# Kernel tuning notes

Hardware: AMD Instinct MI355X
Metric: run time of the kernel (lower is better)

The kernel has to match this reference:

```python
import jax, jax.numpy as jnp
import numpy as np

POOLED_H = 7
POOLED_W = 7
SPATIAL_SCALE = 0.0625
B, C, H, W = 8, 256, 48, 48
R = 300
IMG = 768  # = H / SPATIAL_SCALE


def setup_inputs() -> dict:
    key = jax.random.key(0)
    k1, k2, k3, k4 = jax.random.split(key, 4)
    features = jax.random.normal(k1, (B, C, H, W), dtype=jnp.float32)
    # rois: (batch_idx, x1, y1, x2, y2) in input-image coords
    bidx = jax.random.randint(k2, (R, 1), 0, B).astype(jnp.float32)
    tl = jax.random.uniform(k3, (R, 2), minval=0.0, maxval=IMG - 64.0)
    wh = jax.random.uniform(k4, (R, 2), minval=32.0, maxval=320.0)
    br = jnp.minimum(tl + wh, IMG - 1.0)
    rois = jnp.concatenate([bidx, tl, br], axis=1).astype(jnp.float32)
    return {"features": features, "rois": rois}


def _hat_integral(x, grid):
    """Integral from -inf to x of the unit hat basis function centered at each
    grid point g (support [g-1, g+1], peak 1, total mass 1).
    x: [..., 1-broadcastable], grid: [G] -> returns [..., G]."""
    t = x[..., None] - (grid - 1.0)
    return jnp.where(
        t <= 0.0, 0.0,
        jnp.where(t <= 1.0, 0.5 * t * t,
                  jnp.where(t <= 2.0, 1.0 - 0.5 * (2.0 - t) ** 2, 1.0)))


def reference(features, rois):
    # Precise RoI Pooling: exact double integral of the bilinear interpolant
    # over each bin, divided by bin area. Bilinear interp (with zero padding
    # outside the map, as in the CUDA PrRoIPoolingGetData) is
    #   f(u,v) = sum_{j,i} feat[j,i] * hat_j(v) * hat_i(u)
    # so the bin integral factorizes into per-axis hat-integral weights.
    Bf, Cf, Hf, Wf = features.shape
    bidx = rois[:, 0].astype(jnp.int32)
    x1 = rois[:, 1] * SPATIAL_SCALE
    y1 = rois[:, 2] * SPATIAL_SCALE
    x2 = rois[:, 3] * SPATIAL_SCALE
    y2 = rois[:, 4] * SPATIAL_SCALE
    roi_w = jnp.maximum(x2 - x1, 0.0)
    roi_h = jnp.maximum(y2 - y1, 0.0)
    bin_w = roi_w / POOLED_W  # [R]
    bin_h = roi_h / POOLED_H

    ph = jnp.arange(POOLED_H, dtype=jnp.float32)
    pw = jnp.arange(POOLED_W, dtype=jnp.float32)
    ya = y1[:, None] + ph[None, :] * bin_h[:, None]  # [R, PH]
    yb = ya + bin_h[:, None]
    xa = x1[:, None] + pw[None, :] * bin_w[:, None]  # [R, PW]
    xb = xa + bin_w[:, None]

    gy = jnp.arange(Hf, dtype=jnp.float32)
    gx = jnp.arange(Wf, dtype=jnp.float32)
    Wy = _hat_integral(yb, gy) - _hat_integral(ya, gy)  # [R, PH, H]
    Wx = _hat_integral(xb, gx) - _hat_integral(xa, gx)  # [R, PW, W]

    feat = features[bidx]  # [R, C, H, W]
    t = jnp.einsum('rpj,rcji->rcpi', Wy, feat)   # integrate over y
    num = jnp.einsum('rqi,rcpi->rcpq', Wx, t)    # integrate over x -> [R,C,PH,PW]

    area = (bin_w * bin_h)[:, None, None, None]  # win_size per ROI
    out = jnp.where(area > 0.0, num / jnp.where(area > 0.0, area, 1.0), 0.0)
    return out
```

## Files before the change

kernel.cpp:

```cpp
#include <hip/hip_runtime.h>


#define PH 7
#define PW 7
#define NBINS 49
#define SCALE 0.0625f
#define CH 256
#define FH 48
#define FW 48
#define RNUM 300
#define PATCHF (23 * 56)
#define RSF 328

__device__ __forceinline__ float hat_int(float x, float g) {
    float t = x - (g - 1.0f);
    if (t <= 0.0f) return 0.0f;
    if (t <= 1.0f) return 0.5f * t * t;
    if (t <= 2.0f) { float u = 2.0f - t; return 1.0f - 0.5f * u * u; }
    return 1.0f;
}

__global__ __launch_bounds__(256, 6)
void prroi_one(const float* __restrict__ feat,
               const float* __restrict__ rois,
               float* __restrict__ out) {
    const int wv   = threadIdx.x >> 6;
    const int lane = threadIdx.x & 63;
    const int r    = blockIdx.y;
    const int cpr  = blockIdx.x * 4 + wv;
    const int c0   = cpr * 2;

    __shared__ float lds[4][PATCHF + RSF];
    float* patch = lds[wv];
    float* rsw   = lds[wv] + PATCHF;

    const float* roi = rois + r * 5;
    const float f0 = roi[0], f1 = roi[1], f2 = roi[2], f3 = roi[3], f4 = roi[4];
    const int   b  = (int)f0;
    const float x1 = f1 * SCALE, y1 = f2 * SCALE;
    const float x2 = f3 * SCALE, y2 = f4 * SCALE;
    const float roi_w = fmaxf(x2 - x1, 0.0f), roi_h = fmaxf(y2 - y1, 0.0f);
    const float bin_w = roi_w / (float)PW, bin_h = roi_h / (float)PH;
    const float area = bin_w * bin_h;
    const float ia   = (area > 0.0f) ? (1.0f / area) : 0.0f;

    const float ylo = fminf(y1, y2), yhi = fmaxf(y1, y2);
    const float xlo = fminf(x1, x2), xhi = fmaxf(x1, x2);
    const int j1 = min(FH - 1, (int)floorf(yhi) + 1);
    const int i1 = min(FW - 1, (int)floorf(xhi) + 1);
    const int J0 = min(max(0, (int)floorf(ylo) - 1), FH - 6);
    const int I0 = min(max(0, (int)floorf(xlo) - 1) & ~3, FW - 8);
    const int JROWS = min(FH - J0, max(j1 - J0 + 1, 6));
    int NI4 = min(((i1 - I0) >> 2) + 1, (FW - I0) >> 2);
    NI4 = max(NI4, 2);

    const int NU = JROWS << 3;
    const float* fb = feat + (size_t)(b * CH + c0) * (FH * FW);
    bool act_[3]; int dst_[3];
    float4 pc0[3], pc1[3];
#pragma unroll
    for (int s = 0; s < 3; ++s) {
        const int u  = lane + (s << 6);
        const int j  = u >> 3, i4 = u & 7;
        const bool a = (u < NU) && (i4 < NI4);
        act_[s] = a;
        dst_[s] = j * 56 + 8 * i4;
        if (a) {
            const float* src = fb + (size_t)(J0 + j) * FW + I0 + 4 * i4;
            pc0[s] = *(const float4*)(src);
            pc1[s] = *(const float4*)(src + FH * FW);
        }
    }

    const int  pwA = lane >> 3, jsl = lane & 7;
    const bool actA = lane < 56;
    float wx0 = 0, wx1 = 0, wx2 = 0, wx3 = 0, wx4 = 0, wx5 = 0;
    int biA = 0;
    if (actA) {
        const float xa = x1 + pwA * bin_w, xb = xa + bin_w;
        const int base = min(max((int)floorf(xa) - 1, I0), I0 + 4 * NI4 - 6);
        biA = base - I0;
        wx0 = hat_int(xb, (float)(base + 0)) - hat_int(xa, (float)(base + 0));
        wx1 = hat_int(xb, (float)(base + 1)) - hat_int(xa, (float)(base + 1));
        wx2 = hat_int(xb, (float)(base + 2)) - hat_int(xa, (float)(base + 2));
        wx3 = hat_int(xb, (float)(base + 3)) - hat_int(xa, (float)(base + 3));
        wx4 = hat_int(xb, (float)(base + 4)) - hat_int(xa, (float)(base + 4));
        wx5 = hat_int(xb, (float)(base + 5)) - hat_int(xa, (float)(base + 5));
    }
    const bool actB = lane < NBINS;
    float wy0 = 0, wy1 = 0, wy2 = 0, wy3 = 0, wy4 = 0, wy5 = 0;
    int pwB = 0, bjB = 0;
    if (actB) {
        const int ph = lane / 7;
        pwB = lane - ph * 7;
        const float ya = y1 + ph * bin_h, yb = ya + bin_h;
        const int base = min(max((int)floorf(ya) - 1, J0), J0 + JROWS - 6);
        bjB = base - J0;
        wy0 = hat_int(yb, (float)(base + 0)) - hat_int(ya, (float)(base + 0));
        wy1 = hat_int(yb, (float)(base + 1)) - hat_int(ya, (float)(base + 1));
        wy2 = hat_int(yb, (float)(base + 2)) - hat_int(ya, (float)(base + 2));
        wy3 = hat_int(yb, (float)(base + 3)) - hat_int(ya, (float)(base + 3));
        wy4 = hat_int(yb, (float)(base + 4)) - hat_int(ya, (float)(base + 4));
        wy5 = hat_int(yb, (float)(base + 5)) - hat_int(ya, (float)(base + 5));
    }

#pragma unroll
    for (int s = 0; s < 3; ++s) {
        if (act_[s]) {
            float* d = patch + dst_[s];
            *(float4*)(d + 0) = make_float4(pc0[s].x, pc1[s].x, pc0[s].y, pc1[s].y);
            *(float4*)(d + 4) = make_float4(pc0[s].z, pc1[s].z, pc0[s].w, pc1[s].w);
        }
    }
    asm volatile("s_waitcnt lgkmcnt(0)" ::: "memory");

    if (actA) {
        for (int jr = jsl; jr < JROWS; jr += 8) {
            const float* row = patch + jr * 56 + 2 * biA;
            const float2 v0 = *(const float2*)(row + 0);
            const float2 v1 = *(const float2*)(row + 2);
            const float2 v2 = *(const float2*)(row + 4);
            const float2 v3 = *(const float2*)(row + 6);
            const float2 v4 = *(const float2*)(row + 8);
            const float2 v5 = *(const float2*)(row + 10);
            float ax = 0.0f, ay = 0.0f;
            ax += wx0 * v0.x; ay += wx0 * v0.y;
            ax += wx1 * v1.x; ay += wx1 * v1.y;
            ax += wx2 * v2.x; ay += wx2 * v2.y;
            ax += wx3 * v3.x; ay += wx3 * v3.y;
            ax += wx4 * v4.x; ay += wx4 * v4.y;
            ax += wx5 * v5.x; ay += wx5 * v5.y;
            *(float2*)&rsw[(pwA * 23 + jr) * 2] = make_float2(ax, ay);
        }
    }
    asm volatile("s_waitcnt lgkmcnt(0)" ::: "memory");

    if (actB) {
        const float* rb = rsw + (pwB * 23 + bjB) * 2;
        const float2 u0 = *(const float2*)(rb + 0);
        const float2 u1 = *(const float2*)(rb + 2);
        const float2 u2 = *(const float2*)(rb + 4);
        const float2 u3 = *(const float2*)(rb + 6);
        const float2 u4 = *(const float2*)(rb + 8);
        const float2 u5 = *(const float2*)(rb + 10);
        float ax = 0.0f, ay = 0.0f;
        ax += wy0 * u0.x; ay += wy0 * u0.y;
        ax += wy1 * u1.x; ay += wy1 * u1.y;
        ax += wy2 * u2.x; ay += wy2 * u2.y;
        ax += wy3 * u3.x; ay += wy3 * u3.y;
        ax += wy4 * u4.x; ay += wy4 * u4.y;
        ax += wy5 * u5.x; ay += wy5 * u5.y;
        float* o = out + ((size_t)r * CH + c0) * NBINS + lane;
        o[0]     = ax * ia;
        o[NBINS] = ay * ia;
    }
}

extern "C" void kernel_launch(void* const* d_in, const int* in_sizes, int n_in,
                              void* d_out, int out_size, void* d_ws, size_t ws_size,
                              hipStream_t stream) {
    const float* feat = (const float*)d_in[0];
    const float* rois = (const float*)d_in[1];
    float* out = (float*)d_out;
    (void)d_ws; (void)ws_size;

    prroi_one<<<dim3(32, RNUM), 256, 0, stream>>>(feat, rois, out);
}
```

Baseline: 88.93 us.

## Load feature windows directly from global memory, dropping the LDS patch stage

The per-wave LDS patch staging is removed. Each lane now loads its own 6-wide feature window for up to three rows and two channels straight from global memory using float4+float2 loads, then does the x-integration in registers. This cuts the LDS write, barrier and reread traffic, and shrinks shared memory so the launch bound can rise to 8 blocks per CU. In exchange, adjacent lanes issue overlapping and possibly unaligned global loads that now depend on the L1/L2 caches, and register pressure grows.

```diff
diff --git a/kernel.cpp b/kernel.cpp
--- a/kernel.cpp
+++ b/kernel.cpp
@@ -9,7 +9,6 @@
 #define FH 48
 #define FW 48
 #define RNUM 300
-#define PATCHF (23 * 56)
 #define RSF 328
 
 __device__ __forceinline__ float hat_int(float x, float g) {
@@ -20,19 +19,18 @@
     return 1.0f;
 }
 
-__global__ __launch_bounds__(256, 6)
-void prroi_one(const float* __restrict__ feat,
-               const float* __restrict__ rois,
-               float* __restrict__ out) {
+__global__ __launch_bounds__(256, 8)
+void prroi_direct(const float* __restrict__ feat,
+                  const float* __restrict__ rois,
+                  float* __restrict__ out) {
     const int wv   = threadIdx.x >> 6;
     const int lane = threadIdx.x & 63;
     const int r    = blockIdx.y;
     const int cpr  = blockIdx.x * 4 + wv;
     const int c0   = cpr * 2;
 
-    __shared__ float lds[4][PATCHF + RSF];
-    float* patch = lds[wv];
-    float* rsw   = lds[wv] + PATCHF;
+    __shared__ float rs[4][RSF];
+    float* rsw = rs[wv];
 
     const float* roi = rois + r * 5;
     const float f0 = roi[0], f1 = roi[1], f2 = roi[2], f3 = roi[3], f4 = roi[4];
@@ -54,32 +52,39 @@
     int NI4 = min(((i1 - I0) >> 2) + 1, (FW - I0) >> 2);
     NI4 = max(NI4, 2);
 
-    const int NU = JROWS << 3;
-    const float* fb = feat + (size_t)(b * CH + c0) * (FH * FW);
-    bool act_[3]; int dst_[3];
-    float4 pc0[3], pc1[3];
-#pragma unroll
-    for (int s = 0; s < 3; ++s) {
-        const int u  = lane + (s << 6);
-        const int j  = u >> 3, i4 = u & 7;
-        const bool a = (u < NU) && (i4 < NI4);
-        act_[s] = a;
-        dst_[s] = j * 56 + 8 * i4;
-        if (a) {
-            const float* src = fb + (size_t)(J0 + j) * FW + I0 + 4 * i4;
-            pc0[s] = *(const float4*)(src);
-            pc1[s] = *(const float4*)(src + FH * FW);
-        }
+    const int  pwA = lane >> 3, jsl = lane & 7;
+    const bool actA = lane < 56;
+    int base = I0;
+    float xa = 0.0f, xb = 0.0f;
+    if (actA) {
+        xa = x1 + pwA * bin_w; xb = xa + bin_w;
+        base = min(max((int)floorf(xa) - 1, I0), I0 + 4 * NI4 - 6);
     }
 
-    const int  pwA = lane >> 3, jsl = lane & 7;
-    const bool actA = lane < 56;
+    const float* fb = feat + (size_t)(b * CH + c0) * (FH * FW);
+    const bool m0 = actA && (jsl      < JROWS);
+    const bool m1 = actA && (jsl + 8  < JROWS);
+    const bool m2 = actA && (jsl + 16 < JROWS);
+    const float* p0 = fb + (size_t)(J0 + jsl) * FW + base;
+    float4 a40, b40, a41, b41, a42, b42;
+    float2 a20, b20, a21, b21, a22, b22;
+    if (m0) {
+        a40 = *(const float4*)(p0);            a20 = *(const float2*)(p0 + 4);
+        b40 = *(const float4*)(p0 + FH * FW);  b20 = *(const float2*)(p0 + FH * FW + 4);
+    }
+    if (m1) {
+        const float* p1 = p0 + 8 * FW;
+        a41 = *(const float4*)(p1);            a21 = *(const float2*)(p1 + 4);
+        b41 = *(const float4*)(p1 + FH * FW);  b21 = *(const float2*)(p1 + FH * FW + 4);
+    }
+    if (m2) {
+        const float* p2 = p0 + 16 * FW;
+        a42 = *(const float4*)(p2);            a22 = *(const float2*)(p2 + 4);
+        b42 = *(const float4*)(p2 + FH * FW);  b22 = *(const float2*)(p2 + FH * FW + 4);
+    }
+
     float wx0 = 0, wx1 = 0, wx2 = 0, wx3 = 0, wx4 = 0, wx5 = 0;
-    int biA = 0;
     if (actA) {
-        const float xa = x1 + pwA * bin_w, xb = xa + bin_w;
-        const int base = min(max((int)floorf(xa) - 1, I0), I0 + 4 * NI4 - 6);
-        biA = base - I0;
         wx0 = hat_int(xb, (float)(base + 0)) - hat_int(xa, (float)(base + 0));
         wx1 = hat_int(xb, (float)(base + 1)) - hat_int(xa, (float)(base + 1));
         wx2 = hat_int(xb, (float)(base + 2)) - hat_int(xa, (float)(base + 2));
@@ -94,44 +99,45 @@
         const int ph = lane / 7;
         pwB = lane - ph * 7;
         const float ya = y1 + ph * bin_h, yb = ya + bin_h;
-        const int base = min(max((int)floorf(ya) - 1, J0), J0 + JROWS - 6);
-        bjB = base - J0;
-        wy0 = hat_int(yb, (float)(base + 0)) - hat_int(ya, (float)(base + 0));
-        wy1 = hat_int(yb, (float)(base + 1)) - hat_int(ya, (float)(base + 1));
-        wy2 = hat_int(yb, (float)(base + 2)) - hat_int(ya, (float)(base + 2));
-        wy3 = hat_int(yb, (float)(base + 3)) - hat_int(ya, (float)(base + 3));
-        wy4 = hat_int(yb, (float)(base + 4)) - hat_int(ya, (float)(base + 4));
-        wy5 = hat_int(yb, (float)(base + 5)) - hat_int(ya, (float)(base + 5));
+        const int bs = min(max((int)floorf(ya) - 1, J0), J0 + JROWS - 6);
+        bjB = bs - J0;
+        wy0 = hat_int(yb, (float)(bs + 0)) - hat_int(ya, (float)(bs + 0));
+        wy1 = hat_int(yb, (float)(bs + 1)) - hat_int(ya, (float)(bs + 1));
+        wy2 = hat_int(yb, (float)(bs + 2)) - hat_int(ya, (float)(bs + 2));
+        wy3 = hat_int(yb, (float)(bs + 3)) - hat_int(ya, (float)(bs + 3));
+        wy4 = hat_int(yb, (float)(bs + 4)) - hat_int(ya, (float)(bs + 4));
+        wy5 = hat_int(yb, (float)(bs + 5)) - hat_int(ya, (float)(bs + 5));
     }
 
-#pragma unroll
-    for (int s = 0; s < 3; ++s) {
-        if (act_[s]) {
-            float* d = patch + dst_[s];
-            *(float4*)(d + 0) = make_float4(pc0[s].x, pc1[s].x, pc0[s].y, pc1[s].y);
-            *(float4*)(d + 4) = make_float4(pc0[s].z, pc1[s].z, pc0[s].w, pc1[s].w);
-        }
+    if (m0) {
+        float ax = 0.0f, ay = 0.0f;
+        ax += wx0 * a40.x; ay += wx0 * b40.x;
+        ax += wx1 * a40.y; ay += wx1 * b40.y;
+        ax += wx2 * a40.z; ay += wx2 * b40.z;
+        ax += wx3 * a40.w; ay += wx3 * b40.w;
+        ax += wx4 * a20.x; ay += wx4 * b20.x;
+        ax += wx5 * a20.y; ay += wx5 * b20.y;
+        *(float2*)&rsw[(pwA * 23 + jsl) * 2] = make_float2(ax, ay);
     }
-    asm volatile("s_waitcnt lgkmcnt(0)" ::: "memory");
-
-    if (actA) {
-        for (int jr = jsl; jr < JROWS; jr += 8) {
-            const float* row = patch + jr * 56 + 2 * biA;
-            const float2 v0 = *(const float2*)(row + 0);
-            const float2 v1 = *(const float2*)(row + 2);
-            const float2 v2 = *(const float2*)(row + 4);
-            const float2 v3 = *(const float2*)(row + 6);
-            const float2 v4 = *(const float2*)(row + 8);
-            const float2 v5 = *(const float2*)(row + 10);
-            float ax = 0.0f, ay = 0.0f;
-            ax += wx0 * v0.x; ay += wx0 * v0.y;
-            ax += wx1 * v1.x; ay += wx1 * v1.y;
-            ax += wx2 * v2.x; ay += wx2 * v2.y;
-            ax += wx3 * v3.x; ay += wx3 * v3.y;
-            ax += wx4 * v4.x; ay += wx4 * v4.y;
-            ax += wx5 * v5.x; ay += wx5 * v5.y;
-            *(float2*)&rsw[(pwA * 23 + jr) * 2] = make_float2(ax, ay);
-        }
+    if (m1) {
+        float ax = 0.0f, ay = 0.0f;
+        ax += wx0 * a41.x; ay += wx0 * b41.x;
+        ax += wx1 * a41.y; ay += wx1 * b41.y;
+        ax += wx2 * a41.z; ay += wx2 * b41.z;
+        ax += wx3 * a41.w; ay += wx3 * b41.w;
+        ax += wx4 * a21.x; ay += wx4 * b21.x;
+        ax += wx5 * a21.y; ay += wx5 * b21.y;
+        *(float2*)&rsw[(pwA * 23 + jsl + 8) * 2] = make_float2(ax, ay);
+    }
+    if (m2) {
+        float ax = 0.0f, ay = 0.0f;
+        ax += wx0 * a42.x; ay += wx0 * b42.x;
+        ax += wx1 * a42.y; ay += wx1 * b42.y;
+        ax += wx2 * a42.z; ay += wx2 * b42.z;
+        ax += wx3 * a42.w; ay += wx3 * b42.w;
+        ax += wx4 * a22.x; ay += wx4 * b22.x;
+        ax += wx5 * a22.y; ay += wx5 * b22.y;
+        *(float2*)&rsw[(pwA * 23 + jsl + 16) * 2] = make_float2(ax, ay);
     }
     asm volatile("s_waitcnt lgkmcnt(0)" ::: "memory");
 
@@ -164,5 +170,5 @@
     float* out = (float*)d_out;
     (void)d_ws; (void)ws_size;
 
-    prroi_one<<<dim3(32, RNUM), 256, 0, stream>>>(feat, rois, out);
+    prroi_direct<<<dim3(32, RNUM), 256, 0, stream>>>(feat, rois, out);
 }
```

Measured after the change: 97.59 us. +9.7%, slower.
